# Optimization experiments

Hardware: AMD Instinct MI355X
Metric: run time of the kernel (lower is better)

Reference implementation:

```python
import jax, jax.numpy as jnp
import numpy as np

D_MODEL = 1024
NUM_HEADS = 16
HEAD_DIM = D_MODEL // NUM_HEADS
THETA = 10000.0


def setup_inputs() -> dict:
    key = jax.random.key(0)
    k1, k2, k3 = jax.random.split(key, 3)
    B, S = 4, 2048
    x = jax.random.normal(k1, (B, S, D_MODEL), dtype=jnp.float32)
    token_positions = jnp.arange(S, dtype=jnp.int32)
    std_qkv = 2.0 / (D_MODEL + 3 * D_MODEL)
    std_o = 2.0 / (D_MODEL + D_MODEL)
    W_qkv = jax.random.normal(k2, (3 * D_MODEL, D_MODEL), dtype=jnp.float32) * std_qkv
    W_o = jax.random.normal(k3, (D_MODEL, D_MODEL), dtype=jnp.float32) * std_o
    return {"x": x, "token_positions": token_positions, "W_qkv": W_qkv, "W_o": W_o}


def _apply_rope(x, positions):
    # x: [B, H, S, d]; positions: [S]
    d = x.shape[-1]
    inv_freq = 1.0 / THETA ** (2.0 * jnp.arange(0, d // 2, dtype=jnp.float32) / d)
    angle = positions.astype(jnp.float32)[:, None] * inv_freq[None, :]  # [S, d/2]
    cos, sin = jnp.cos(angle), jnp.sin(angle)
    x1, x2 = x[..., 0::2], x[..., 1::2]
    rot = jnp.stack([x1 * cos - x2 * sin, x2 * cos + x1 * sin], axis=-1)
    return rot.reshape(x.shape)


def reference(x, token_positions, W_qkv, W_o):
    B, S, D = x.shape
    H, hd = NUM_HEADS, HEAD_DIM
    qkv = jnp.einsum('bsi,ji->bsj', x, W_qkv)            # [B, S, 3D]
    qkv = qkv.reshape(B, S, 3, H, hd).transpose(2, 0, 3, 1, 4)  # [3, B, H, S, hd]
    q, k, v = qkv[0], qkv[1], qkv[2]
    q = _apply_rope(q, token_positions)
    k = _apply_rope(k, token_positions)
    scores = jnp.einsum('bhqd,bhkd->bhqk', q, k) / jnp.sqrt(jnp.float32(hd))
    causal = jnp.tril(jnp.ones((S, S), dtype=bool))
    scores = jnp.where(causal, scores, -jnp.inf)
    probs = jax.nn.softmax(scores, axis=-1)
    attn = jnp.einsum('bhqk,bhkd->bhqd', probs, v)       # [B, H, S, hd]
    attn = attn.transpose(0, 2, 1, 3).reshape(B, S, D)
    return jnp.einsum('bsi,ji->bsj', attn, W_o)
```

## Files before the change

kernel.cpp:

```cpp
#include <hip/hip_runtime.h>

#define B_ 4
#define S_ 2048
#define D_ 1024
#define H_ 16
#define HD_ 64
#define M_ (B_*S_)
#define NQKV_ (3*D_)

typedef _Float16 f16;
typedef __attribute__((ext_vector_type(4))) _Float16 f16x4;
typedef __attribute__((ext_vector_type(8))) _Float16 f16x8;
typedef __attribute__((ext_vector_type(4))) float f32x4;
typedef __attribute__((ext_vector_type(16))) float f32x16;
typedef __attribute__((ext_vector_type(2))) int i32x2;
typedef __attribute__((ext_vector_type(4))) int i32x4;

__device__ __forceinline__ void gload_lds16(const void* g, void* lds) {
  __builtin_amdgcn_global_load_lds(
      (const __attribute__((address_space(1))) void*)g,
      (__attribute__((address_space(3))) void*)lds, 16, 0, 0);
}

__global__ void cast3_kernel(const float* __restrict__ x,
                             const float* __restrict__ wqkv,
                             const float* __restrict__ wo,
                             f16* __restrict__ out) {
  size_t gi = (size_t)blockIdx.x * 2048 + (size_t)threadIdx.x * 8;
  const float* src;
  size_t off;
  if (gi < (size_t)M_ * D_)                       { src = x;    off = gi; }
  else if (gi < (size_t)M_ * D_ + (size_t)NQKV_ * D_) { src = wqkv; off = gi - (size_t)M_ * D_; }
  else                                            { src = wo;   off = gi - (size_t)M_ * D_ - (size_t)NQKV_ * D_; }
  float4 a = *reinterpret_cast<const float4*>(src + off);
  float4 b = *reinterpret_cast<const float4*>(src + off + 4);
  f16x8 o;
  o[0] = (f16)a.x; o[1] = (f16)a.y; o[2] = (f16)a.z; o[3] = (f16)a.w;
  o[4] = (f16)b.x; o[5] = (f16)b.y; o[6] = (f16)b.z; o[7] = (f16)b.w;
  *reinterpret_cast<f16x8*>(out + gi) = o;
}

__global__ void trig_kernel(const int* __restrict__ pos, float2* __restrict__ tab) {
  int idx = blockIdx.x * 256 + threadIdx.x;
  int s = idx >> 5, t = idx & 31;
  float p = (float)pos[s];
  float invf = exp2f((float)t * -0.4152410118609203f);
  float sn, cs;
  sincosf(p * invf, &sn, &cs);
  tab[idx] = float2{cs, sn};
}

template <int MODE>
__global__ __launch_bounds__(256, 4)
void gemm_bt(const f16* __restrict__ A, const f16* __restrict__ Bt,
             void* __restrict__ Cout, const float2* __restrict__ tab,
             f16* __restrict__ kout, f16* __restrict__ vtout,
             int M, int N, int K) {
  constexpr int MI = (MODE == 0) ? 4 : 2;
  constexpr int BP = (MODE == 0) ? 2 : 1;
  __shared__ __align__(16) f16 As[2][128 * 32];
  __shared__ __align__(16) f16 Bs[2][BP * 64 * 32];
  const int tid = threadIdx.x;
  const int w = tid >> 6, l = tid & 63;
  const int nM = M >> 7;
  const int bm = (int)(blockIdx.x % nM) << 7;
  const int bn = (int)(blockIdx.x / nM) * (BP * 64);
  const int wrow = (MODE == 0) ? ((w >> 1) << 6) : (w << 5);
  const int wcol = (MODE == 0) ? ((w & 1) << 6) : 0;
  const int lr = l & 15;
  const int lk = (l >> 4) << 3;
  const int orow = (l >> 4) << 2;
  const int swzr = ((lr >> 1) & 3) << 3;
  const int NT = K >> 5;

  f32x4 acc[MI][4];
  #pragma unroll
  for (int i = 0; i < MI; ++i)
    #pragma unroll
    for (int j = 0; j < 4; ++j) acc[i][j] = f32x4{0.f, 0.f, 0.f, 0.f};

  const int srow4 = tid >> 2;
  const int ssw = ((tid & 3) * 8) ^ (((srow4 >> 1) & 3) << 3);

#define STAGE(t_) do {                                                    \
    const int buf_ = (t_) & 1; const int k0_ = (t_) << 5;                 \
    _Pragma("unroll")                                                     \
    for (int p = 0; p < 2; ++p)                                           \
      gload_lds16(A + (size_t)(bm + p * 64 + srow4) * K + k0_ + ssw,      \
                  (void*)(&As[buf_][(p * 256 + tid) * 8]));               \
    _Pragma("unroll")                                                     \
    for (int p = 0; p < BP; ++p)                                          \
      gload_lds16(Bt + (size_t)(bn + p * 64 + srow4) * K + k0_ + ssw,     \
                  (void*)(&Bs[buf_][(p * 256 + tid) * 8]));               \
  } while (0)

  STAGE(0);

  for (int t = 0; t < NT; ++t) {
    if (t + 1 < NT) {
      STAGE(t + 1);
      if constexpr (MODE == 0)
        asm volatile("s_waitcnt vmcnt(4)" ::: "memory");
      else
        asm volatile("s_waitcnt vmcnt(3)" ::: "memory");
    } else {
      asm volatile("s_waitcnt vmcnt(0)" ::: "memory");
    }
    __builtin_amdgcn_sched_barrier(0);
    __builtin_amdgcn_s_barrier();
    __builtin_amdgcn_sched_barrier(0);

    const f16* Asc = As[t & 1];
    const f16* Bsc = Bs[t & 1];
    f16x8 af[MI], bf[4];
    #pragma unroll
    for (int mi = 0; mi < MI; ++mi)
      af[mi] = *reinterpret_cast<const f16x8*>(
          Asc + (wrow + mi * 16 + lr) * 32 + (lk ^ swzr));
    #pragma unroll
    for (int ni = 0; ni < 4; ++ni)
      bf[ni] = *reinterpret_cast<const f16x8*>(
          Bsc + (wcol + ni * 16 + lr) * 32 + (lk ^ swzr));
    #pragma unroll
    for (int mi = 0; mi < MI; ++mi)
      #pragma unroll
      for (int ni = 0; ni < 4; ++ni)
        acc[mi][ni] = __builtin_amdgcn_mfma_f32_16x16x32_f16(bf[ni], af[mi], acc[mi][ni], 0, 0, 0);

    __builtin_amdgcn_sched_barrier(0);
    __builtin_amdgcn_s_barrier();
    __builtin_amdgcn_sched_barrier(0);
  }
#undef STAGE

  if (MODE == 0) {
    const int which = bn >> 10;
    const int h = ((bn + wcol) >> 6) & (H_ - 1);
    if (which < 2) {
      f16* dst = which ? kout : (f16*)Cout;
      const float qs = which ? 1.0f : 0.125f * 1.4426950408889634f;
      #pragma unroll
      for (int mi = 0; mi < MI; ++mi) {
        int m = bm + wrow + mi * 16 + lr;
        int b = m >> 11, s = m & (S_ - 1);
        size_t rowbase = ((size_t)(b * H_ + h) * S_ + s) * HD_;
        const float4* trow = reinterpret_cast<const float4*>(tab + (size_t)s * 32);
        #pragma unroll
        for (int ni = 0; ni < 4; ++ni) {
          int d0 = ni * 16 + orow;
          float4 cssn = trow[d0 >> 2];
          float x0 = acc[mi][ni][0], x1 = acc[mi][ni][1];
          float x2 = acc[mi][ni][2], x3 = acc[mi][ni][3];
          f16x4 ov;
          ov[0] = (f16)((x0 * cssn.x - x1 * cssn.y) * qs);
          ov[1] = (f16)((x1 * cssn.x + x0 * cssn.y) * qs);
          ov[2] = (f16)((x2 * cssn.z - x3 * cssn.w) * qs);
          ov[3] = (f16)((x3 * cssn.z + x2 * cssn.w) * qs);
          *reinterpret_cast<f16x4*>(&dst[rowbase + d0]) = ov;
        }
      }
    } else {
      #pragma unroll
      for (int mi = 0; mi < MI; ++mi) {
        int m = bm + wrow + mi * 16 + lr;
        int b = m >> 11, s = m & (S_ - 1);
        size_t base = (size_t)(b * H_ + h) * (HD_ * S_) + s;
        #pragma unroll
        for (int ni = 0; ni < 4; ++ni)
          #pragma unroll
          for (int r = 0; r < 4; ++r)
            vtout[base + (size_t)(ni * 16 + orow + r) * S_] = (f16)acc[mi][ni][r];
      }
    }
  } else {
    float* C = (float*)Cout;
    #pragma unroll
    for (int mi = 0; mi < MI; ++mi) {
      int m = bm + wrow + mi * 16 + lr;
      #pragma unroll
      for (int ni = 0; ni < 4; ++ni) {
        int n = bn + wcol + ni * 16 + orow;
        *reinterpret_cast<float4*>(&C[(size_t)m * N + n]) =
            float4{acc[mi][ni][0], acc[mi][ni][1], acc[mi][ni][2], acc[mi][ni][3]};
      }
    }
  }
}

__global__ __launch_bounds__(256, 4)
void attn_kernel(const f16* __restrict__ q, const f16* __restrict__ k,
                 const f16* __restrict__ vt, f16* __restrict__ attn_out) {
  __shared__ __align__(16) f16 Ks[64 * 64];
  __shared__ __align__(16) f16 Vs[64 * 64];
  const int tid = threadIdx.x, wq = tid >> 6, l = tid & 63;
  const int lq = l & 31, hi = l >> 5;
  const int bh = blockIdx.x & 63;
  const int qt = 15 - (int)(blockIdx.x >> 6);
  const int q0 = qt << 7;
  const size_t bhoff = (size_t)bh * (S_ * HD_);
  const size_t vtoff = (size_t)bh * (HD_ * S_);
  const int srow = tid >> 3;
  const int sc8 = (tid & 7) * 8;
  const int ssw = sc8 ^ ((srow & 7) << 3);
  const int swz = (lq & 7) << 3;
  const int h = bh & (H_ - 1), b = bh >> 4;
  const int wqmin = q0 + wq * 32;
  const int qrow = wqmin + lq;

  f16x8 qf[4];
  #pragma unroll
  for (int s = 0; s < 4; ++s)
    qf[s] = *reinterpret_cast<const f16x8*>(q + bhoff + (size_t)qrow * HD_ + s * 16 + hi * 8);

  f32x16 o[2];
  float m_run = -1e30f, l_run = 0.f;
  #pragma unroll
  for (int i = 0; i < 2; ++i)
    #pragma unroll
    for (int r = 0; r < 16; ++r) o[i][r] = 0.f;

  const int ntiles = 2 * qt + 2;
  for (int it = 0; it < ntiles; ++it) {
    const int kv0 = it << 6;
    __syncthreads();
    #pragma unroll
    for (int i = 0; i < 2; ++i) {
      gload_lds16(k + bhoff + (size_t)(kv0 + i * 32 + srow) * HD_ + ssw,
                  (void*)(Ks + (i * 256 + wq * 64) * 8));
      gload_lds16(vt + vtoff + (size_t)(i * 32 + srow) * S_ + kv0 + ssw,
                  (void*)(Vs + (i * 256 + wq * 64) * 8));
    }
    __syncthreads();

    if (kv0 <= wqmin + 31) {
      f32x16 sacc[2];
      #pragma unroll
      for (int kh = 0; kh < 2; ++kh) {
        #pragma unroll
        for (int r = 0; r < 16; ++r) sacc[kh][r] = 0.f;
        #pragma unroll
        for (int s = 0; s < 4; ++s) {
          f16x8 kf = *reinterpret_cast<const f16x8*>(
              Ks + (kh * 32 + lq) * 64 + ((s * 16 + hi * 8) ^ swz));
          sacc[kh] = __builtin_amdgcn_mfma_f32_32x32x16_f16(kf, qf[s], sacc[kh], 0, 0, 0);
        }
      }
      if (kv0 + 63 >= wqmin) {
        #pragma unroll
        for (int kh = 0; kh < 2; ++kh)
          #pragma unroll
          for (int r = 0; r < 16; ++r) {
            int kvg = kv0 + kh * 32 + (r & 3) + 8 * (r >> 2) + 4 * hi;
            if (kvg > qrow) sacc[kh][r] = -1e30f;
          }
      }

      float mloc = -1e30f;
      #pragma unroll
      for (int kh = 0; kh < 2; ++kh)
        #pragma unroll
        for (int r = 0; r < 16; ++r) mloc = fmaxf(mloc, sacc[kh][r]);
      mloc = fmaxf(mloc, __shfl_xor(mloc, 32));
      if (__any(mloc > m_run + 8.f)) {
        float mn = fmaxf(m_run, mloc);
        float scale = exp2f(m_run - mn);
        m_run = mn;
        l_run *= scale;
        #pragma unroll
        for (int i = 0; i < 2; ++i)
          #pragma unroll
          for (int r = 0; r < 16; ++r) o[i][r] *= scale;
      }
      float sloc = 0.f;
      #pragma unroll
      for (int kh = 0; kh < 2; ++kh)
        #pragma unroll
        for (int r = 0; r < 16; ++r) {
          sacc[kh][r] = exp2f(sacc[kh][r] - m_run);
          sloc += sacc[kh][r];
        }
      sloc += __shfl_xor(sloc, 32);
      l_run += sloc;

      f16x8 pf[4];
      #pragma unroll
      for (int ks = 0; ks < 4; ++ks) {
        const int khh = ks >> 1;
        f16x4 pA, pB;
        #pragma unroll
        for (int r = 0; r < 4; ++r) {
          pA[r] = (f16)sacc[khh][(ks & 1) * 8 + r];
          pB[r] = (f16)sacc[khh][(ks & 1) * 8 + 4 + r];
        }
        i32x2 ia = __builtin_bit_cast(i32x2, pA);
        i32x2 ib = __builtin_bit_cast(i32x2, pB);
        i32x2 oth, rcv, lo2, hh2;
        oth.x = hi ? ia.x : ib.x;
        oth.y = hi ? ia.y : ib.y;
        rcv.x = __shfl_xor(oth.x, 32);
        rcv.y = __shfl_xor(oth.y, 32);
        lo2.x = hi ? rcv.x : ia.x;
        lo2.y = hi ? rcv.y : ia.y;
        hh2.x = hi ? ib.x : rcv.x;
        hh2.y = hi ? ib.y : rcv.y;
        i32x4 full{lo2.x, lo2.y, hh2.x, hh2.y};
        pf[ks] = __builtin_bit_cast(f16x8, full);
      }

      #pragma unroll
      for (int dh = 0; dh < 2; ++dh)
        #pragma unroll
        for (int s2 = 0; s2 < 4; ++s2) {
          f16x8 vf = *reinterpret_cast<const f16x8*>(
              Vs + (dh * 32 + lq) * 64 + ((s2 * 16 + hi * 8) ^ swz));
          o[dh] = __builtin_amdgcn_mfma_f32_32x32x16_f16(vf, pf[s2], o[dh], 0, 0, 0);
        }
    }
  }

  float rl = 1.0f / l_run;
  #pragma unroll
  for (int dh = 0; dh < 2; ++dh)
    #pragma unroll
    for (int qd = 0; qd < 4; ++qd) {
      f16x4 ov;
      #pragma unroll
      for (int r = 0; r < 4; ++r) ov[r] = (f16)(o[dh][qd * 4 + r] * rl);
      int d0 = dh * 32 + qd * 8 + hi * 4;
      *reinterpret_cast<f16x4*>(
          &attn_out[(size_t)(b * S_ + qrow) * D_ + h * HD_ + d0]) = ov;
    }
}

extern "C" void kernel_launch(void* const* d_in, const int* in_sizes, int n_in,
                              void* d_out, int out_size, void* d_ws, size_t ws_size,
                              hipStream_t stream) {
  const float* x    = (const float*)d_in[0];
  const int*   pos  = (const int*)d_in[1];
  const float* wqkv = (const float*)d_in[2];
  const float* wo   = (const float*)d_in[3];
  float* out = (float*)d_out;

  const size_t BHSD = (size_t)B_ * H_ * S_ * HD_;
  f16* xb    = (f16*)d_ws;
  f16* wqkvb = xb + (size_t)M_ * D_;
  f16* wob   = wqkvb + (size_t)NQKV_ * D_;
  f16* qb    = wob + (size_t)D_ * D_;
  f16* kb    = qb + BHSD;
  f16* vtb   = kb + BHSD;
  f16* attnb = vtb + BHSD;
  float2* tab = (float2*)(attnb + BHSD);

  cast3_kernel<<<6144, 256, 0, stream>>>(x, wqkv, wo, xb);
  trig_kernel<<<(S_ * 32) / 256, 256, 0, stream>>>(pos, tab);

  gemm_bt<0><<<(M_ / 128) * (NQKV_ / 128), 256, 0, stream>>>(
      xb, wqkvb, (void*)qb, tab, kb, vtb, M_, NQKV_, D_);

  attn_kernel<<<64 * 16, 256, 0, stream>>>(qb, kb, vtb, attnb);

  gemm_bt<1><<<(M_ / 128) * (D_ / 64), 256, 0, stream>>>(
      attnb, wob, (void*)out, nullptr, nullptr, nullptr, M_, D_, D_);
}
```

Before: 181.5 us.

## Double-buffer K/V tiles in attention kernel with async LDS prefetch

Gives the K and V shared-memory tiles two buffers and issues the global-to-LDS load for the next KV tile before computing on the current one. Explicit vmcnt waits and barriers replace the two __syncthreads per iteration, so load latency can overlap with the MFMA and softmax work. LDS use doubles to 32KB per block, which may limit occupancy against the launch bound of 4 blocks. Correctness now depends on the manual vmcnt count matching the four outstanding loads.

New measurement: 182.4 us. No clear change (+0.5%).

```diff
diff --git a/kernel.cpp b/kernel.cpp
--- a/kernel.cpp
+++ b/kernel.cpp
@@ -190,8 +190,8 @@
 __global__ __launch_bounds__(256, 4)
 void attn_kernel(const f16* __restrict__ q, const f16* __restrict__ k,
                  const f16* __restrict__ vt, f16* __restrict__ attn_out) {
-  __shared__ __align__(16) f16 Ks[64 * 64];
-  __shared__ __align__(16) f16 Vs[64 * 64];
+  __shared__ __align__(16) f16 Ks[2][64 * 64];
+  __shared__ __align__(16) f16 Vs[2][64 * 64];
   const int tid = threadIdx.x, wq = tid >> 6, l = tid & 63;
   const int lq = l & 31, hi = l >> 5;
   const int bh = blockIdx.x & 63;
@@ -220,17 +220,34 @@
     for (int r = 0; r < 16; ++r) o[i][r] = 0.f;
 
   const int ntiles = 2 * qt + 2;
+
+#define ASTAGE(t_) do {                                                   \
+    const int buf_ = (t_) & 1; const int kv_ = (t_) << 6;                 \
+    _Pragma("unroll")                                                     \
+    for (int i = 0; i < 2; ++i) {                                         \
+      gload_lds16(k + bhoff + (size_t)(kv_ + i * 32 + srow) * HD_ + ssw,  \
+                  (void*)(&Ks[buf_][(i * 256 + wq * 64) * 8]));           \
+      gload_lds16(vt + vtoff + (size_t)(i * 32 + srow) * S_ + kv_ + ssw,  \
+                  (void*)(&Vs[buf_][(i * 256 + wq * 64) * 8]));           \
+    }                                                                     \
+  } while (0)
+
+  ASTAGE(0);
+
   for (int it = 0; it < ntiles; ++it) {
     const int kv0 = it << 6;
-    __syncthreads();
-    #pragma unroll
-    for (int i = 0; i < 2; ++i) {
-      gload_lds16(k + bhoff + (size_t)(kv0 + i * 32 + srow) * HD_ + ssw,
-                  (void*)(Ks + (i * 256 + wq * 64) * 8));
-      gload_lds16(vt + vtoff + (size_t)(i * 32 + srow) * S_ + kv0 + ssw,
-                  (void*)(Vs + (i * 256 + wq * 64) * 8));
-    }
-    __syncthreads();
+    if (it + 1 < ntiles) {
+      ASTAGE(it + 1);
+      asm volatile("s_waitcnt vmcnt(4)" ::: "memory");
+    } else {
+      asm volatile("s_waitcnt vmcnt(0)" ::: "memory");
+    }
+    __builtin_amdgcn_sched_barrier(0);
+    __builtin_amdgcn_s_barrier();
+    __builtin_amdgcn_sched_barrier(0);
+
+    const f16* Ksc = Ks[it & 1];
+    const f16* Vsc = Vs[it & 1];
 
     if (kv0 <= wqmin + 31) {
       f32x16 sacc[2];
@@ -241,7 +258,7 @@
         #pragma unroll
         for (int s = 0; s < 4; ++s) {
           f16x8 kf = *reinterpret_cast<const f16x8*>(
-              Ks + (kh * 32 + lq) * 64 + ((s * 16 + hi * 8) ^ swz));
+              Ksc + (kh * 32 + lq) * 64 + ((s * 16 + hi * 8) ^ swz));
           sacc[kh] = __builtin_amdgcn_mfma_f32_32x32x16_f16(kf, qf[s], sacc[kh], 0, 0, 0);
         }
       }
@@ -312,11 +329,16 @@
         #pragma unroll
         for (int s2 = 0; s2 < 4; ++s2) {
           f16x8 vf = *reinterpret_cast<const f16x8*>(
-              Vs + (dh * 32 + lq) * 64 + ((s2 * 16 + hi * 8) ^ swz));
+              Vsc + (dh * 32 + lq) * 64 + ((s2 * 16 + hi * 8) ^ swz));
           o[dh] = __builtin_amdgcn_mfma_f32_32x32x16_f16(vf, pf[s2], o[dh], 0, 0, 0);
         }
     }
+
+    __builtin_amdgcn_sched_barrier(0);
+    __builtin_amdgcn_s_barrier();
+    __builtin_amdgcn_sched_barrier(0);
   }
+#undef ASTAGE
 
   float rl = 1.0f / l_run;
   #pragma unroll
```

## Split attention KV range into two chunks and merge partial softmax outputs

Applied to the files above, without the earlier changes.

Each query tile's key/value range is split into two halves handled by separate blocks, which doubles the grid from 1024 to 2048 blocks and evens out the causal load imbalance. Each half writes a normalized partial output plus its running max and sum, and a new merge kernel combines the halves with log-sum-exp weights. Freed workspace buffers (the x and W_qkv casts) are reused to hold the partials. The cost is an extra kernel launch and an extra pass over the attention output, plus rounding the partials to f16 before the merge.

Result: slower. 188.6 us (+3.9%).

```diff
diff --git a/kernel.cpp b/kernel.cpp
--- a/kernel.cpp
+++ b/kernel.cpp
@@ -189,14 +189,20 @@
 
 __global__ __launch_bounds__(256, 4)
 void attn_kernel(const f16* __restrict__ q, const f16* __restrict__ k,
-                 const f16* __restrict__ vt, f16* __restrict__ attn_out) {
+                 const f16* __restrict__ vt,
+                 f16* __restrict__ oA, f16* __restrict__ oB,
+                 float2* __restrict__ mlA, float2* __restrict__ mlB) {
   __shared__ __align__(16) f16 Ks[64 * 64];
   __shared__ __align__(16) f16 Vs[64 * 64];
   const int tid = threadIdx.x, wq = tid >> 6, l = tid & 63;
   const int lq = l & 31, hi = l >> 5;
   const int bh = blockIdx.x & 63;
-  const int qt = 15 - (int)(blockIdx.x >> 6);
+  const int rest = (int)(blockIdx.x >> 6);
+  const int chunk = rest & 1;
+  const int qt = 15 - (rest >> 1);
   const int q0 = qt << 7;
+  const int it0 = chunk ? (qt + 1) : 0;
+  const int it1 = chunk ? (2 * qt + 2) : (qt + 1);
   const size_t bhoff = (size_t)bh * (S_ * HD_);
   const size_t vtoff = (size_t)bh * (HD_ * S_);
   const int srow = tid >> 3;
@@ -219,8 +225,7 @@
     #pragma unroll
     for (int r = 0; r < 16; ++r) o[i][r] = 0.f;
 
-  const int ntiles = 2 * qt + 2;
-  for (int it = 0; it < ntiles; ++it) {
+  for (int it = it0; it < it1; ++it) {
     const int kv0 = it << 6;
     __syncthreads();
     #pragma unroll
@@ -318,7 +323,8 @@
     }
   }
 
-  float rl = 1.0f / l_run;
+  f16* dst = chunk ? oB : oA;
+  float rl = (l_run > 0.f) ? (1.0f / l_run) : 0.f;
   #pragma unroll
   for (int dh = 0; dh < 2; ++dh)
     #pragma unroll
@@ -328,8 +334,35 @@
       for (int r = 0; r < 4; ++r) ov[r] = (f16)(o[dh][qd * 4 + r] * rl);
       int d0 = dh * 32 + qd * 8 + hi * 4;
       *reinterpret_cast<f16x4*>(
-          &attn_out[(size_t)(b * S_ + qrow) * D_ + h * HD_ + d0]) = ov;
-    }
+          &dst[(size_t)(b * S_ + qrow) * D_ + h * HD_ + d0]) = ov;
+    }
+  if (hi == 0) {
+    float2* ml = chunk ? mlB : mlA;
+    ml[((b * H_ + h) << 11) + qrow] = float2{m_run, l_run};
+  }
+}
+
+__global__ void merge_kernel(const f16* __restrict__ oA, const f16* __restrict__ oB,
+                             const float2* __restrict__ mlA, const float2* __restrict__ mlB,
+                             f16* __restrict__ out) {
+  size_t addr = ((size_t)blockIdx.x * 256 + threadIdx.x) * 8;
+  int hh = (int)((addr >> 6) & 15);
+  int ss = (int)((addr >> 10) & 2047);
+  int bb = (int)(addr >> 21);
+  int mlidx = ((bb * H_ + hh) << 11) + ss;
+  float2 a = mlA[mlidx], c = mlB[mlidx];
+  float m = fmaxf(a.x, c.x);
+  float sA = exp2f(a.x - m) * a.y;
+  float sB = exp2f(c.x - m) * c.y;
+  float inv = 1.0f / (sA + sB);
+  float wA = sA * inv, wB = sB * inv;
+  f16x8 va = *reinterpret_cast<const f16x8*>(oA + addr);
+  f16x8 vb = *reinterpret_cast<const f16x8*>(oB + addr);
+  f16x8 o;
+  #pragma unroll
+  for (int j = 0; j < 8; ++j)
+    o[j] = (f16)(wA * (float)va[j] + wB * (float)vb[j]);
+  *reinterpret_cast<f16x8*>(out + addr) = o;
 }
 
 extern "C" void kernel_launch(void* const* d_in, const int* in_sizes, int n_in,
@@ -350,6 +383,9 @@
   f16* vtb   = kb + BHSD;
   f16* attnb = vtb + BHSD;
   float2* tab = (float2*)(attnb + BHSD);
+  f16* oB = xb;
+  float2* mlA = (float2*)wqkvb;
+  float2* mlB = mlA + (size_t)B_ * H_ * S_;
 
   cast3_kernel<<<6144, 256, 0, stream>>>(x, wqkv, wo, xb);
   trig_kernel<<<(S_ * 32) / 256, 256, 0, stream>>>(pos, tab);
@@ -357,7 +393,8 @@
   gemm_bt<0><<<(M_ / 128) * (NQKV_ / 128), 256, 0, stream>>>(
       xb, wqkvb, (void*)qb, tab, kb, vtb, M_, NQKV_, D_);
 
-  attn_kernel<<<64 * 16, 256, 0, stream>>>(qb, kb, vtb, attnb);
+  attn_kernel<<<64 * 32, 256, 0, stream>>>(qb, kb, vtb, attnb, oB, mlA, mlB);
+  merge_kernel<<<(int)(BHSD / 8 / 256), 256, 0, stream>>>(attnb, oB, mlA, mlB, attnb);
 
   gemm_bt<1><<<(M_ / 128) * (D_ / 64), 256, 0, stream>>>(
       attnb, wob, (void*)out, nullptr, nullptr, nullptr, M_, D_, D_);
```
